# Optimization experiments

Hardware: AMD Instinct MI355X
Metric: run time of the kernel (lower is better)

## Reference

```python
import jax, jax.numpy as jnp
import numpy as np

H, U = 64, 64  # matrix-completion patch size; system size is (H*U)^2 = 4096^2


def svtC(X, tau):
    # Singular value thresholding: soft-threshold singular values by tau.
    u, s, vt = jnp.linalg.svd(X, full_matrices=False)
    return (u * jax.nn.relu(s - tau)) @ vt


def setup_inputs() -> dict:
    key = jax.random.key(0)
    ks = jax.random.split(key, 12)
    x = jax.random.normal(ks[0], (H, U), jnp.float32)
    L = jax.random.normal(ks[1], (H, U), jnp.float32)
    entries_mask = jax.random.randint(ks[2], (H, U), 0, 2).astype(bool)
    # D_tilda: symmetric PSD (HU, HU) smoothness operator so the system is well-conditioned
    M = jax.random.normal(ks[3], (H * U, H * U), jnp.float32)
    D_tilda = (M @ M.T) / jnp.float32(H * U)
    th_P = jax.random.normal(ks[4], (H, U), jnp.float32)
    v = jax.random.normal(ks[5], (), jnp.float32)
    coef_gamma = jax.random.uniform(ks[6], (), jnp.float32)
    neta = jax.random.uniform(ks[7], (), jnp.float32)
    lamda1 = jax.random.uniform(ks[8], (), jnp.float32)
    lamda2 = jax.random.uniform(ks[9], (), jnp.float32)
    rho = jax.random.uniform(ks[10], (), jnp.float32) + jnp.float32(0.1)
    S = jax.random.normal(ks[11], (H, H), jnp.float32) / np.float32(np.sqrt(H))
    return {"x": x, "L": L, "entries_mask": entries_mask, "D_tilda": D_tilda,
            "th_P": th_P, "v": v, "coef_gamma": coef_gamma, "neta": neta,
            "lamda1": lamda1, "lamda2": lamda2, "rho": rho, "S": S}


def reference(x, L, entries_mask, D_tilda, th_P, v, coef_gamma, neta,
              lamda1, lamda2, rho, S):
    tau = jax.nn.sigmoid(v) * coef_gamma
    # Q_tilda = diag(vec(mask)); S_tilda = kron(I_U, S^T S)
    q = entries_mask.astype(jnp.float32).reshape(-1)  # (HU,)
    StS = S.T @ S                                      # (H, H)
    S_tilda = jnp.kron(jnp.eye(U, dtype=jnp.float32), StS)  # (HU, HU)
    eye = jnp.eye(H * U, dtype=jnp.float32)
    A = jnp.diag(q) + lamda1 * D_tilda + lamda2 * S_tilda + rho * eye
    vec = rho * (L - th_P) + jnp.where(entries_mask, x, jnp.float32(0.0))
    # Original uses explicit dense inverse followed by matvec
    Xtmp = (jnp.linalg.inv(A) @ vec.reshape(-1)).reshape(H, U)
    Ltmp = svtC(Xtmp + th_P, tau)
    Ptmp = th_P + neta * (Xtmp - Ltmp)
    return Ltmp, Ptmp
```

## Files before the change

kernel.cpp:

```cpp
#include <hip/hip_runtime.h>
#include <cstddef>

#define HU    4096
#define NBLK  256
#define NTHR  512
#define MAXIT 100
#define TOL2  1e-7f

#define WS_STS  0
#define WS_DINV 4096
#define WS_R0   8192
#define WS_U0   12288
#define WS_W    16384
#define WS_DEL  24576
#define WS_BAR  (WS_DEL + (MAXIT + 2) * 64)
#define WS_FLAG (WS_BAR + 8 * 16)
#define WS_END  (WS_FLAG + 8 * 16)

typedef _Float16 half4v __attribute__((ext_vector_type(4)));

__device__ __forceinline__ float fastrcp(float x) {
  float r; asm("v_rcp_f32 %0, %1" : "=v"(r) : "v"(x)); return r;
}
__device__ __forceinline__ float fastsqrt(float x) {
  float r; asm("v_sqrt_f32 %0, %1" : "=v"(r) : "v"(x)); return r;
}
__device__ __forceinline__ float fastrsq(float x) {
  float r; asm("v_rsq_f32 %0, %1" : "=v"(r) : "v"(x)); return r;
}

__device__ __forceinline__ float waveReduce(float v) {
#pragma unroll
  for (int off = 32; off > 0; off >>= 1) v += __shfl_xor(v, off, 64);
  return v;
}

__device__ __forceinline__ float blockSum(float v, float* red) {
  v = waveReduce(v);
  if ((threadIdx.x & 63) == 0) red[threadIdx.x >> 6] = v;
  __syncthreads();
  float s = 0.f;
#pragma unroll
  for (int i = 0; i < 8; ++i) s += red[i];
  __syncthreads();
  return s;
}

__device__ __forceinline__ void gsync_init(unsigned* cnt, unsigned* flg, unsigned gen) {
  __syncthreads();
  if (threadIdx.x == 0) {
    __threadfence();
    __hip_atomic_fetch_add(&cnt[(blockIdx.x & 7) * 16], 1u,
                           __ATOMIC_RELEASE, __HIP_MEMORY_SCOPE_AGENT);
    if (blockIdx.x == 0) {
      const unsigned target = gen * NBLK;
      for (;;) {
        unsigned s = 0;
#pragma unroll
        for (int i = 0; i < 8; ++i)
          s += __hip_atomic_load(&cnt[i * 16], __ATOMIC_RELAXED, __HIP_MEMORY_SCOPE_AGENT);
        if (s >= target) break;
      }
#pragma unroll
      for (int i = 0; i < 8; ++i)
        __hip_atomic_store(&flg[i * 16], gen, __ATOMIC_RELEASE, __HIP_MEMORY_SCOPE_AGENT);
    } else {
      const int fl = (blockIdx.x & 7) * 16;
      while (__hip_atomic_load(&flg[fl], __ATOMIC_RELAXED, __HIP_MEMORY_SCOPE_AGENT) < gen)
        __builtin_amdgcn_s_sleep(1);
    }
    __threadfence();
  }
  __syncthreads();
}

__device__ __forceinline__ float gsync_dk(unsigned* cnt, unsigned* flg, unsigned gen,
                                          float* dslot, float* redf) {
  __syncthreads();
  const int b = blockIdx.x;
  if (b == 0) {
    if (threadIdx.x < 64) {
      if (threadIdx.x == 0) {
        __threadfence();
        __hip_atomic_fetch_add(&cnt[0], 1u, __ATOMIC_RELEASE, __HIP_MEMORY_SCOPE_AGENT);
        const unsigned target = gen * NBLK;
        for (;;) {
          unsigned s = 0;
#pragma unroll
          for (int i = 0; i < 8; ++i)
            s += __hip_atomic_load(&cnt[i * 16], __ATOMIC_RELAXED, __HIP_MEMORY_SCOPE_AGENT);
          if (s >= target) break;
        }
        __threadfence();
      }
      const float dv = __hip_atomic_load(&dslot[threadIdx.x],
                                         __ATOMIC_RELAXED, __HIP_MEMORY_SCOPE_AGENT);
      const float dk = waveReduce(dv);
      if (threadIdx.x == 0) {
        const unsigned bits = __float_as_uint(dk);
#pragma unroll
        for (int i = 0; i < 8; ++i) {
          __hip_atomic_store(&flg[i * 16 + 1], bits, __ATOMIC_RELAXED, __HIP_MEMORY_SCOPE_AGENT);
          __hip_atomic_store(&flg[i * 16],    gen,  __ATOMIC_RELEASE, __HIP_MEMORY_SCOPE_AGENT);
        }
        redf[0] = dk;
      }
    }
  } else {
    if (threadIdx.x == 0) {
      __threadfence();
      __hip_atomic_fetch_add(&cnt[(b & 7) * 16], 1u,
                             __ATOMIC_RELEASE, __HIP_MEMORY_SCOPE_AGENT);
      const int fl = (b & 7) * 16;
      while (__hip_atomic_load(&flg[fl], __ATOMIC_RELAXED, __HIP_MEMORY_SCOPE_AGENT) < gen)
        __builtin_amdgcn_s_sleep(1);
      const unsigned bits = __hip_atomic_load(&flg[fl + 1],
                                              __ATOMIC_RELAXED, __HIP_MEMORY_SCOPE_AGENT);
      __threadfence();
      redf[0] = __uint_as_float(bits);
    }
  }
  __syncthreads();
  const float dk = redf[0];
  __syncthreads();
  return dk;
}

#define SWP 6
#define S_W 68

__device__ __forceinline__ float red16(float x) {
  int t;
  t = __builtin_amdgcn_update_dpp(0, __float_as_int(x), 0x128, 0xF, 0xF, false);
  x += __int_as_float(t);
  t = __builtin_amdgcn_update_dpp(0, __float_as_int(x), 0x124, 0xF, 0xF, false);
  x += __int_as_float(t);
  t = __builtin_amdgcn_update_dpp(0, __float_as_int(x), 0x122, 0xF, 0xF, false);
  x += __int_as_float(t);
  t = __builtin_amdgcn_update_dpp(0, __float_as_int(x), 0x121, 0xF, 0xF, false);
  x += __int_as_float(t);
  return x;
}

__global__ void __launch_bounds__(NTHR, 1)
fused_kernel(const float* __restrict__ x_in, const float* __restrict__ L_in,
             const int* __restrict__ mask, const float* __restrict__ D,
             const float* __restrict__ thP, const float* __restrict__ S,
             const float* __restrict__ l1p, const float* __restrict__ l2p,
             const float* __restrict__ rhop, const float* __restrict__ vp,
             const float* __restrict__ cgp, const float* __restrict__ netap,
             float* __restrict__ ws, float* __restrict__ out)
{
  __shared__ __align__(16) float u_l[HU];
  __shared__ __align__(16) char pool[128 * 1024];
  __shared__ float red[8];
  __shared__ float g_s[64];
  unsigned* cnt  = (unsigned*)(ws + WS_BAR);
  unsigned* flg  = (unsigned*)(ws + WS_FLAG);
  const float* sts = ws + WS_STS;
  const float lam1 = *l1p, lam2 = *l2p, rho = *rhop;
  const int tid = threadIdx.x, b = blockIdx.x;
  const int wv = tid >> 6, lane = tid & 63;
  unsigned gen = 0;

  const int gtid = b * NTHR + tid;
  if (gtid < HU) {
    const int a = gtid >> 6, c = gtid & 63;
    float acc = 0.f, sdiag = 0.f;
    for (int h = 0; h < 64; ++h) {
      const float sa = S[h * 64 + a], sc = S[h * 64 + c];
      acc = fmaf(sa, sc, acc);
      sdiag = fmaf(sc, sc, sdiag);
    }
    ws[WS_STS + gtid] = acc;
    const float q = mask[gtid] ? 1.f : 0.f;
    const float diag = q + rho + lam1 * D[(size_t)gtid * (HU + 1)] + lam2 * sdiag;
    const float bb = rho * (L_in[gtid] - thP[gtid]) + (mask[gtid] ? x_in[gtid] : 0.f);
    const float di = 1.f / diag;
    ws[WS_DINV + gtid] = di;
    ws[WS_R0 + gtid] = bb;
    ws[WS_U0 + gtid] = bb * di;
  }

  {
    const float4* __restrict__ Dg = (const float4*)(D + (size_t)b * 16 * HU);
    half4v* __restrict__ Dh4 = (half4v*)pool;
    for (int o = tid; o < 16 * HU / 4; o += NTHR) {
      const float4 dv = Dg[o];
      half4v h;
      h[0] = (_Float16)dv.x; h[1] = (_Float16)dv.y;
      h[2] = (_Float16)dv.z; h[3] = (_Float16)dv.w;
      Dh4[o] = h;
    }
  }
  gsync_init(cnt, flg, ++gen);

  float r_reg[8], s_reg[8], dinv_reg[8];
  float acc0 = 0.f;
#pragma unroll
  for (int m = 0; m < 8; ++m) {
    const int i = tid + m * NTHR;
    const float rv = ws[WS_R0 + i], uv = ws[WS_U0 + i];
    r_reg[m] = rv; u_l[i] = uv; dinv_reg[m] = ws[WS_DINV + i];
    s_reg[m] = 0.f;
  }
  __syncthreads();
#pragma unroll
  for (int m = 0; m < 8; ++m) acc0 = fmaf(r_reg[m], u_l[tid + m * NTHR], acc0);
  const float gamma0 = blockSum(acc0, red);

  float p_arr[8], x_arr[8];
#pragma unroll
  for (int m = 0; m < 8; ++m) { p_arr[m] = 0.f; x_arr[m] = 0.f; }

  const int row0 = b * 16 + wv * 2;
  const int iq = row0 >> 6, j0 = row0 & 63;
  const float4* __restrict__ u4 = (const float4*)u_l;
  const float m0 = mask[row0] ? 1.f : 0.f;
  const float m1 = mask[row0 + 1] ? 1.f : 0.f;
  const float sts0 = sts[j0 * 64 + lane];
  const float sts1 = sts[j0 * 64 + 64 + lane];
  const float dex0 = D[(size_t)row0 * (HU + 1)];
  const float dex1 = D[(size_t)(row0 + 1) * (HU + 1)];
  const float diagf0 = m0 + rho + lam1 * (dex0 - (float)(_Float16)dex0);
  const float diagf1 = m1 + rho + lam1 * (dex1 - (float)(_Float16)dex1);
  const half4v* __restrict__ H0 = (const half4v*)((_Float16*)pool + (size_t)(wv * 2) * HU);
  const half4v* __restrict__ H1 = H0 + (HU / 4);

  float gamma = gamma0, gamma_prev = 1.f, alpha_prev = 1.f;
  for (int k = 0; k < MAXIT; ++k) {
    float* __restrict__ wbuf = ws + WS_W + (k & 1) * HU;
    {
      float acc_a = 0.f, acc_b = 0.f;
#pragma unroll
      for (int it = 0; it < 16; ++it) {
        const float4 uu = u4[it * 64 + lane];
        const half4v d0 = H0[it * 64 + lane];
        const half4v d1 = H1[it * 64 + lane];
        acc_a = fmaf((float)d0[0], uu.x, acc_a); acc_a = fmaf((float)d0[1], uu.y, acc_a);
        acc_a = fmaf((float)d0[2], uu.z, acc_a); acc_a = fmaf((float)d0[3], uu.w, acc_a);
        acc_b = fmaf((float)d1[0], uu.x, acc_b); acc_b = fmaf((float)d1[1], uu.y, acc_b);
        acc_b = fmaf((float)d1[2], uu.z, acc_b); acc_b = fmaf((float)d1[3], uu.w, acc_b);
      }
      const float us = u_l[iq * 64 + lane];
      float t0 = fmaf(lam1, acc_a, lam2 * (sts0 * us));
      float t1 = fmaf(lam1, acc_b, lam2 * (sts1 * us));
      t0 = waveReduce(t0);
      t1 = waveReduce(t1);
      const float u0v = u_l[row0], u1v = u_l[row0 + 1];
      const float w0 = t0 + diagf0 * u0v;
      const float w1 = t1 + diagf1 * u1v;
      if (lane == 0) {
        wbuf[row0] = w0;
        wbuf[row0 + 1] = w1;
        red[wv] = fmaf(w0, u0v, w1 * u1v);
      }
      __syncthreads();
      if (tid == 0) {
        float s = 0.f;
#pragma unroll
        for (int k2 = 0; k2 < 8; ++k2) s += red[k2];
        atomicAdd(&ws[WS_DEL + k * 64 + (b & 63)], s);
      }
    }
    const float dk = gsync_dk(cnt, flg, ++gen, ws + WS_DEL + k * 64, red);

    const float beta  = (k == 0) ? 0.f : gamma * fastrcp(gamma_prev);
    const float denom = (k == 0) ? dk  : (dk - beta * gamma * fastrcp(alpha_prev));
    const float alpha = gamma * fastrcp(denom);

    float acc = 0.f;
#pragma unroll
    for (int m = 0; m < 8; ++m) {
      const int i = tid + m * NTHR;
      const float uold = u_l[i];
      const float wvv = wbuf[i];
      const float sv = (k == 0) ? wvv : fmaf(beta, s_reg[m], wvv);
      s_reg[m] = sv;
      const float rv = fmaf(-alpha, sv, r_reg[m]);
      r_reg[m] = rv;
      const float uv = rv * dinv_reg[m];
      u_l[i] = uv;
      acc = fmaf(rv, uv, acc);
      const float pk = (k == 0) ? uold : fmaf(beta, p_arr[m], uold);
      p_arr[m] = pk;
      x_arr[m] = fmaf(alpha, pk, x_arr[m]);
    }
    const float gnext = blockSum(acc, red);

    gamma_prev = gamma;
    alpha_prev = alpha;
    gamma = gnext;
    if (!(gnext > TOL2 * gamma0)) break;
  }

  if (b != 0) return;

  float* Wl = (float*)pool;
  float* Yr = Wl + 64 * S_W;
  float* T1 = Yr + 64 * S_W;
  float* Wr = T1 + 64 * S_W;
  __syncthreads();

  float t0acc = 0.f;
#pragma unroll
  for (int mm = 0; mm < 8; ++mm) {
    const int i = tid + mm * NTHR;
    const int rr = i >> 6, cc = i & 63;
    const float y = x_arr[mm] + thP[i];
    Wl[cc * S_W + rr] = y;
    Yr[rr * S_W + cc] = y;
    t0acc = fmaf(y, y, t0acc);
  }
  const float T0 = blockSum(t0acc, red);
  const float thr = 1.6e-10f * T0 * T0;

  const int pid = tid >> 4;
  const int sub = tid & 15;
  int p = (pid == 0) ? 63 : pid;
  int q = (pid == 0) ? 0  : 63 - pid;

  for (int sweep = 0; sweep < SWP; ++sweep) {
    float offacc = 0.f;
    for (int rnd = 0; rnd < 63; ++rnd) {
      float4* wp = (float4*)(Wl + p * S_W) + sub;
      float4* wq = (float4*)(Wl + q * S_W) + sub;
      const float4 a = *wp, bb = *wq;
      float dpp = fmaf(a.x, a.x, fmaf(a.y, a.y, fmaf(a.z, a.z, a.w * a.w)));
      float dqq = fmaf(bb.x, bb.x, fmaf(bb.y, bb.y, fmaf(bb.z, bb.z, bb.w * bb.w)));
      float dpq = fmaf(a.x, bb.x, fmaf(a.y, bb.y, fmaf(a.z, bb.z, a.w * bb.w)));
      dpp = red16(dpp); dqq = red16(dqq); dpq = red16(dpq);
      offacc = fmaf(dpq, dpq, offacc);
      if (dpq * dpq > 1e-14f * dpp * dqq) {
        const float th = (dqq - dpp) * 0.5f * fastrcp(dpq);
        const float sg = (th >= 0.f) ? 1.f : -1.f;
        const float t  = sg * fastrcp(fabsf(th) + fastsqrt(fmaf(th, th, 1.f)));
        const float c1 = fastrsq(fmaf(t, t, 1.f));
        const float s1 = t * c1;
        float4 na, nb;
        na.x = c1 * a.x - s1 * bb.x;  nb.x = s1 * a.x + c1 * bb.x;
        na.y = c1 * a.y - s1 * bb.y;  nb.y = s1 * a.y + c1 * bb.y;
        na.z = c1 * a.z - s1 * bb.z;  nb.z = s1 * a.z + c1 * bb.z;
        na.w = c1 * a.w - s1 * bb.w;  nb.w = s1 * a.w + c1 * bb.w;
        *wp = na; *wq = nb;
      }
      if (pid) { p = (p + 1 == 63) ? 0 : p + 1; }
      q = (q + 1 == 63) ? 0 : q + 1;
      __syncthreads();
    }
    const float tot = blockSum(offacc, red);
    if (sweep >= 2 && tot < thr) break;
  }

  if (tid < 64) {
    const float4* wc = (const float4*)(Wl + tid * S_W);
    float nn = 0.f;
#pragma unroll
    for (int i2 = 0; i2 < 16; ++i2) {
      const float4 u = wc[i2];
      nn = fmaf(u.x, u.x, fmaf(u.y, u.y, fmaf(u.z, u.z, fmaf(u.w, u.w, nn))));
    }
    const float sv = sqrtf(nn);
    const float tau = (*cgp) / (1.f + expf(-(*vp)));
    g_s[tid] = (sv > tau) ? (sv - tau) / (sv * nn) : 0.f;
  }
  __syncthreads();

  const int j = tid & 63;
  const int ib = tid >> 6;

#pragma unroll
  for (int mm = 0; mm < 8; ++mm) {
    const int k = ib + 8 * mm;
    const float4* wcol = (const float4*)(Wl + k * S_W);
    float acc = 0.f;
#pragma unroll
    for (int i4 = 0; i4 < 16; ++i4) {
      const float4 wvv = wcol[i4];
      acc = fmaf(wvv.x, Yr[(4 * i4 + 0) * S_W + j], acc);
      acc = fmaf(wvv.y, Yr[(4 * i4 + 1) * S_W + j], acc);
      acc = fmaf(wvv.z, Yr[(4 * i4 + 2) * S_W + j], acc);
      acc = fmaf(wvv.w, Yr[(4 * i4 + 3) * S_W + j], acc);
    }
    T1[k * S_W + j] = acc;
  }
  for (int o = tid; o < 4096; o += 512) {
    const int i2 = o >> 6, kk = o & 63;
    Wr[i2 * S_W + kk] = Wl[kk * S_W + i2] * g_s[kk];
  }
  __syncthreads();

  const float neta = *netap;
#pragma unroll
  for (int mm = 0; mm < 8; ++mm) {
    const int i2 = ib + 8 * mm;
    const float4* wrow = (const float4*)(Wr + i2 * S_W);
    float acc = 0.f;
#pragma unroll
    for (int k4 = 0; k4 < 16; ++k4) {
      const float4 wvv = wrow[k4];
      acc = fmaf(wvv.x, T1[(4 * k4 + 0) * S_W + j], acc);
      acc = fmaf(wvv.y, T1[(4 * k4 + 1) * S_W + j], acc);
      acc = fmaf(wvv.z, T1[(4 * k4 + 2) * S_W + j], acc);
      acc = fmaf(wvv.w, T1[(4 * k4 + 3) * S_W + j], acc);
    }
    const int o = i2 * 64 + j;
    out[o] = acc;
    out[4096 + o] = thP[o] + neta * (x_arr[mm] - acc);
  }
}

extern "C" void kernel_launch(void* const* d_in, const int* in_sizes, int n_in,
                              void* d_out, int out_size, void* d_ws, size_t ws_size,
                              hipStream_t stream)
{
  const float* x_in  = (const float*)d_in[0];
  const float* L_in  = (const float*)d_in[1];
  const int*   mask  = (const int*)d_in[2];
  const float* D     = (const float*)d_in[3];
  const float* thP   = (const float*)d_in[4];
  const float* vp    = (const float*)d_in[5];
  const float* cgp   = (const float*)d_in[6];
  const float* netap = (const float*)d_in[7];
  const float* l1p   = (const float*)d_in[8];
  const float* l2p   = (const float*)d_in[9];
  const float* rhop  = (const float*)d_in[10];
  const float* S     = (const float*)d_in[11];
  float* ws  = (float*)d_ws;
  float* out = (float*)d_out;

  hipMemsetAsync(ws + WS_DEL, 0, (WS_END - WS_DEL) * sizeof(float), stream);

  void* args[] = { (void*)&x_in, (void*)&L_in, (void*)&mask, (void*)&D, (void*)&thP,
                   (void*)&S, (void*)&l1p, (void*)&l2p, (void*)&rhop,
                   (void*)&vp, (void*)&cgp, (void*)&netap, (void*)&ws, (void*)&out };
  hipLaunchCooperativeKernel((void*)fused_kernel, dim3(NBLK), dim3(NTHR),
                             args, 0, stream);
}
```

Measured before the change: 382.2 us.

## Restructure grid barrier and Jacobi SVD ordering to cut block-wide syncs

The grid barrier now spreads arrival counters over 32 slots that a whole wave of block 0 polls in parallel. The dk reduction moves out of the barrier: every block reads the 64 partial sums after the barrier and reduces them itself, instead of block 0 broadcasting the value through the flags. The one-sided Jacobi SVD replaces the 63-round round-robin schedule, which needed a __syncthreads per round, with a GF(8)-based block ordering. Each wave handles an 8-column group for 7 rounds with no block barrier, so there are only 9 block syncs per sweep. This trades barrier latency for more index arithmetic, and the different rotation order may change convergence behaviour.

```diff
diff --git a/kernel.cpp b/kernel.cpp
--- a/kernel.cpp
+++ b/kernel.cpp
@@ -6,6 +6,7 @@
 #define NTHR  512
 #define MAXIT 100
 #define TOL2  1e-7f
+#define NARR  32
 
 #define WS_STS  0
 #define WS_DINV 4096
@@ -14,7 +15,7 @@
 #define WS_W    16384
 #define WS_DEL  24576
 #define WS_BAR  (WS_DEL + (MAXIT + 2) * 64)
-#define WS_FLAG (WS_BAR + 8 * 16)
+#define WS_FLAG (WS_BAR + NARR * 16)
 #define WS_END  (WS_FLAG + 8 * 16)
 
 typedef _Float16 half4v __attribute__((ext_vector_type(4)));
@@ -32,6 +33,11 @@
 __device__ __forceinline__ float waveReduce(float v) {
 #pragma unroll
   for (int off = 32; off > 0; off >>= 1) v += __shfl_xor(v, off, 64);
+  return v;
+}
+__device__ __forceinline__ unsigned waveReduceU(unsigned v) {
+#pragma unroll
+  for (int off = 32; off > 0; off >>= 1) v += __shfl_xor((int)v, off, 64);
   return v;
 }
 
@@ -46,36 +52,7 @@
   return s;
 }
 
-__device__ __forceinline__ void gsync_init(unsigned* cnt, unsigned* flg, unsigned gen) {
-  __syncthreads();
-  if (threadIdx.x == 0) {
-    __threadfence();
-    __hip_atomic_fetch_add(&cnt[(blockIdx.x & 7) * 16], 1u,
-                           __ATOMIC_RELEASE, __HIP_MEMORY_SCOPE_AGENT);
-    if (blockIdx.x == 0) {
-      const unsigned target = gen * NBLK;
-      for (;;) {
-        unsigned s = 0;
-#pragma unroll
-        for (int i = 0; i < 8; ++i)
-          s += __hip_atomic_load(&cnt[i * 16], __ATOMIC_RELAXED, __HIP_MEMORY_SCOPE_AGENT);
-        if (s >= target) break;
-      }
-#pragma unroll
-      for (int i = 0; i < 8; ++i)
-        __hip_atomic_store(&flg[i * 16], gen, __ATOMIC_RELEASE, __HIP_MEMORY_SCOPE_AGENT);
-    } else {
-      const int fl = (blockIdx.x & 7) * 16;
-      while (__hip_atomic_load(&flg[fl], __ATOMIC_RELAXED, __HIP_MEMORY_SCOPE_AGENT) < gen)
-        __builtin_amdgcn_s_sleep(1);
-    }
-    __threadfence();
-  }
-  __syncthreads();
-}
-
-__device__ __forceinline__ float gsync_dk(unsigned* cnt, unsigned* flg, unsigned gen,
-                                          float* dslot, float* redf) {
+__device__ __forceinline__ void gsync(unsigned* cnt, unsigned* flg, unsigned gen) {
   __syncthreads();
   const int b = blockIdx.x;
   if (b == 0) {
@@ -83,47 +60,30 @@
       if (threadIdx.x == 0) {
         __threadfence();
         __hip_atomic_fetch_add(&cnt[0], 1u, __ATOMIC_RELEASE, __HIP_MEMORY_SCOPE_AGENT);
-        const unsigned target = gen * NBLK;
-        for (;;) {
-          unsigned s = 0;
-#pragma unroll
-          for (int i = 0; i < 8; ++i)
-            s += __hip_atomic_load(&cnt[i * 16], __ATOMIC_RELAXED, __HIP_MEMORY_SCOPE_AGENT);
-          if (s >= target) break;
-        }
-        __threadfence();
-      }
-      const float dv = __hip_atomic_load(&dslot[threadIdx.x],
-                                         __ATOMIC_RELAXED, __HIP_MEMORY_SCOPE_AGENT);
-      const float dk = waveReduce(dv);
-      if (threadIdx.x == 0) {
-        const unsigned bits = __float_as_uint(dk);
-#pragma unroll
-        for (int i = 0; i < 8; ++i) {
-          __hip_atomic_store(&flg[i * 16 + 1], bits, __ATOMIC_RELAXED, __HIP_MEMORY_SCOPE_AGENT);
-          __hip_atomic_store(&flg[i * 16],    gen,  __ATOMIC_RELEASE, __HIP_MEMORY_SCOPE_AGENT);
-        }
-        redf[0] = dk;
-      }
-    }
-  } else {
-    if (threadIdx.x == 0) {
+      }
+      const unsigned target = gen * NBLK;
+      for (;;) {
+        unsigned s = (threadIdx.x < NARR)
+          ? __hip_atomic_load(&cnt[threadIdx.x * 16], __ATOMIC_RELAXED, __HIP_MEMORY_SCOPE_AGENT)
+          : 0u;
+        if (waveReduceU(s) >= target) break;
+        __builtin_amdgcn_s_sleep(1);
+      }
       __threadfence();
-      __hip_atomic_fetch_add(&cnt[(b & 7) * 16], 1u,
-                             __ATOMIC_RELEASE, __HIP_MEMORY_SCOPE_AGENT);
-      const int fl = (b & 7) * 16;
-      while (__hip_atomic_load(&flg[fl], __ATOMIC_RELAXED, __HIP_MEMORY_SCOPE_AGENT) < gen)
-        __builtin_amdgcn_s_sleep(1);
-      const unsigned bits = __hip_atomic_load(&flg[fl + 1],
-                                              __ATOMIC_RELAXED, __HIP_MEMORY_SCOPE_AGENT);
-      __threadfence();
-      redf[0] = __uint_as_float(bits);
-    }
-  }
-  __syncthreads();
-  const float dk = redf[0];
-  __syncthreads();
-  return dk;
+      if (threadIdx.x < 8)
+        __hip_atomic_store(&flg[threadIdx.x * 16], gen,
+                           __ATOMIC_RELEASE, __HIP_MEMORY_SCOPE_AGENT);
+    }
+  } else if (threadIdx.x == 0) {
+    __threadfence();
+    __hip_atomic_fetch_add(&cnt[(b & (NARR - 1)) * 16], 1u,
+                           __ATOMIC_RELEASE, __HIP_MEMORY_SCOPE_AGENT);
+    const int fl = (b & 7) * 16;
+    while (__hip_atomic_load(&flg[fl], __ATOMIC_RELAXED, __HIP_MEMORY_SCOPE_AGENT) < gen)
+      __builtin_amdgcn_s_sleep(1);
+    __threadfence();
+  }
+  __syncthreads();
 }
 
 #define SWP 6
@@ -140,6 +100,28 @@
   t = __builtin_amdgcn_update_dpp(0, __float_as_int(x), 0x121, 0xF, 0xF, false);
   x += __int_as_float(t);
   return x;
+}
+
+__device__ __forceinline__ int gf8mul(int a, int b) {
+  int p = 0;
+  if (b & 1) p ^= a;
+  if (b & 2) p ^= (a << 1);
+  if (b & 4) p ^= (a << 2);
+  if (p & 16) p ^= 22;
+  if (p & 8)  p ^= 11;
+  return p;
+}
+
+__device__ __forceinline__ int sel8(const int c[8], int i) {
+  int r = c[0];
+  r = (i == 1) ? c[1] : r;
+  r = (i == 2) ? c[2] : r;
+  r = (i == 3) ? c[3] : r;
+  r = (i == 4) ? c[4] : r;
+  r = (i == 5) ? c[5] : r;
+  r = (i == 6) ? c[6] : r;
+  r = (i == 7) ? c[7] : r;
+  return r;
 }
 
 __global__ void __launch_bounds__(NTHR, 1)
@@ -193,7 +175,7 @@
       Dh4[o] = h;
     }
   }
-  gsync_init(cnt, flg, ++gen);
+  gsync(cnt, flg, ++gen);
 
   float r_reg[8], s_reg[8], dinv_reg[8];
   float acc0 = 0.f;
@@ -263,7 +245,17 @@
         atomicAdd(&ws[WS_DEL + k * 64 + (b & 63)], s);
       }
     }
-    const float dk = gsync_dk(cnt, flg, ++gen, ws + WS_DEL + k * 64, red);
+    gsync(cnt, flg, ++gen);
+
+    if (wv == 0) {
+      const float dv = __hip_atomic_load(&ws[WS_DEL + k * 64 + lane],
+                                         __ATOMIC_RELAXED, __HIP_MEMORY_SCOPE_AGENT);
+      const float w = waveReduce(dv);
+      if (lane == 0) red[0] = w;
+    }
+    __syncthreads();
+    const float dk = red[0];
+    __syncthreads();
 
     const float beta  = (k == 0) ? 0.f : gamma * fastrcp(gamma_prev);
     const float denom = (k == 0) ? dk  : (dk - beta * gamma * fastrcp(alpha_prev));
@@ -315,37 +307,43 @@
   const float T0 = blockSum(t0acc, red);
   const float thr = 1.6e-10f * T0 * T0;
 
-  const int pid = tid >> 4;
-  const int sub = tid & 15;
-  int p = (pid == 0) ? 63 : pid;
-  int q = (pid == 0) ? 0  : 63 - pid;
+  const int team = lane >> 4;
+  const int sub  = lane & 15;
 
   for (int sweep = 0; sweep < SWP; ++sweep) {
     float offacc = 0.f;
-    for (int rnd = 0; rnd < 63; ++rnd) {
-      float4* wp = (float4*)(Wl + p * S_W) + sub;
-      float4* wq = (float4*)(Wl + q * S_W) + sub;
-      const float4 a = *wp, bb = *wq;
-      float dpp = fmaf(a.x, a.x, fmaf(a.y, a.y, fmaf(a.z, a.z, a.w * a.w)));
-      float dqq = fmaf(bb.x, bb.x, fmaf(bb.y, bb.y, fmaf(bb.z, bb.z, bb.w * bb.w)));
-      float dpq = fmaf(a.x, bb.x, fmaf(a.y, bb.y, fmaf(a.z, bb.z, a.w * bb.w)));
-      dpp = red16(dpp); dqq = red16(dqq); dpq = red16(dpq);
-      offacc = fmaf(dpq, dpq, offacc);
-      if (dpq * dpq > 1e-14f * dpp * dqq) {
-        const float th = (dqq - dpp) * 0.5f * fastrcp(dpq);
-        const float sg = (th >= 0.f) ? 1.f : -1.f;
-        const float t  = sg * fastrcp(fabsf(th) + fastsqrt(fmaf(th, th, 1.f)));
-        const float c1 = fastrsq(fmaf(t, t, 1.f));
-        const float s1 = t * c1;
-        float4 na, nb;
-        na.x = c1 * a.x - s1 * bb.x;  nb.x = s1 * a.x + c1 * bb.x;
-        na.y = c1 * a.y - s1 * bb.y;  nb.y = s1 * a.y + c1 * bb.y;
-        na.z = c1 * a.z - s1 * bb.z;  nb.z = s1 * a.z + c1 * bb.z;
-        na.w = c1 * a.w - s1 * bb.w;  nb.w = s1 * a.w + c1 * bb.w;
-        *wp = na; *wq = nb;
-      }
-      if (pid) { p = (p + 1 == 63) ? 0 : p + 1; }
-      q = (q + 1 == 63) ? 0 : q + 1;
+    for (int mr = 0; mr < 9; ++mr) {
+      int cols[8];
+#pragma unroll
+      for (int j = 0; j < 8; ++j)
+        cols[j] = (mr == 8) ? (8 * wv + j) : (8 * j + (gf8mul(mr, j) ^ wv));
+      for (int r = 0; r < 7; ++r) {
+        const int pi = (team == 0) ? 7 : ((r + team) % 7);
+        const int qi = (team == 0) ? (r % 7) : ((r + 7 - team) % 7);
+        const int cp = sel8(cols, pi);
+        const int cq = sel8(cols, qi);
+        float4* wp = (float4*)(Wl + cp * S_W) + sub;
+        float4* wq = (float4*)(Wl + cq * S_W) + sub;
+        const float4 a = *wp, bb = *wq;
+        float dpp = fmaf(a.x, a.x, fmaf(a.y, a.y, fmaf(a.z, a.z, a.w * a.w)));
+        float dqq = fmaf(bb.x, bb.x, fmaf(bb.y, bb.y, fmaf(bb.z, bb.z, bb.w * bb.w)));
+        float dpq = fmaf(a.x, bb.x, fmaf(a.y, bb.y, fmaf(a.z, bb.z, a.w * bb.w)));
+        dpp = red16(dpp); dqq = red16(dqq); dpq = red16(dpq);
+        offacc = fmaf(dpq, dpq, offacc);
+        if (dpq * dpq > 1e-14f * dpp * dqq) {
+          const float th = (dqq - dpp) * 0.5f * fastrcp(dpq);
+          const float sg = (th >= 0.f) ? 1.f : -1.f;
+          const float t  = sg * fastrcp(fabsf(th) + fastsqrt(fmaf(th, th, 1.f)));
+          const float c1 = fastrsq(fmaf(t, t, 1.f));
+          const float s1 = t * c1;
+          float4 na, nb;
+          na.x = c1 * a.x - s1 * bb.x;  nb.x = s1 * a.x + c1 * bb.x;
+          na.y = c1 * a.y - s1 * bb.y;  nb.y = s1 * a.y + c1 * bb.y;
+          na.z = c1 * a.z - s1 * bb.z;  nb.z = s1 * a.z + c1 * bb.z;
+          na.w = c1 * a.w - s1 * bb.w;  nb.w = s1 * a.w + c1 * bb.w;
+          *wp = na; *wq = nb;
+        }
+      }
       __syncthreads();
     }
     const float tot = blockSum(offacc, red);
```

Measured after the change: 332.6 us. 1.15x faster.
